# Optimization experiments

Measured on AMD Instinct MI355X. Metric: run time of the kernel, lower is better.

Reference implementation:

```python
import jax, jax.numpy as jnp
import numpy as np

D = 256  # hardcoded Dense units in the original layer

def setup_inputs() -> dict:
    key = jax.random.key(0)
    ks = jax.random.split(key, 7)
    B, S, F = 8, 2048, 256
    x = jax.random.normal(ks[0], (B, S, F), dtype=jnp.float32)
    # Dense layers (kernel + bias), glorot-ish scale
    scale = 1.0 / np.sqrt(F)
    Wq = jax.random.normal(ks[1], (F, D), dtype=jnp.float32) * scale
    Wk = jax.random.normal(ks[2], (F, D), dtype=jnp.float32) * scale
    Wv = jax.random.normal(ks[3], (F, D), dtype=jnp.float32) * scale
    bq = jax.random.normal(ks[4], (D,), dtype=jnp.float32) * 0.01
    bk = jax.random.normal(ks[5], (D,), dtype=jnp.float32) * 0.01
    bv = jax.random.normal(ks[6], (D,), dtype=jnp.float32) * 0.01
    return {"x": x, "Wq": Wq, "bq": bq, "Wk": Wk, "bk": bk, "Wv": Wv, "bv": bv}

def reference(x, Wq, bq, Wk, bk, Wv, bv):
    # Q/K/V projections: Dense(256) == x @ W + b
    Q = jnp.einsum('bsf,fd->bsd', x, Wq) + bq
    K = jnp.einsum('bsf,fd->bsd', x, Wk) + bk
    V = jnp.einsum('bsf,fd->bsd', x, Wv) + bv
    scores = jnp.einsum('bqd,bkd->bqk', Q, K) / jnp.sqrt(jnp.float32(D))
    attn = jax.nn.softmax(scores, axis=-1)
    return jnp.einsum('bqk,bkd->bqd', attn, V)
```

## Files before the change

kernel.cpp:

```cpp
#include <hip/hip_runtime.h>

typedef __bf16 bf16;
typedef __bf16 bf16x4v __attribute__((ext_vector_type(4)));
typedef __bf16 bf16x8 __attribute__((ext_vector_type(8)));
typedef float f32x4 __attribute__((ext_vector_type(4)));
typedef short s16x4 __attribute__((ext_vector_type(4)));

#define MFMA_X32(A, B, C) __builtin_amdgcn_mfma_f32_16x16x32_bf16(A, B, C, 0, 0, 0)

#if __has_builtin(__builtin_amdgcn_mfma_f32_16x16x16_bf16)
static __device__ __forceinline__ f32x4 mfma_x16(bf16x4v a, bf16x4v b, f32x4 c) {
  return __builtin_amdgcn_mfma_f32_16x16x16_bf16(a, b, c, 0, 0, 0);
}
#else
static __device__ __forceinline__ f32x4 mfma_x16(bf16x4v a, bf16x4v b, f32x4 c) {
  return __builtin_amdgcn_mfma_f32_16x16x16bf16_1k(
      __builtin_bit_cast(s16x4, a), __builtin_bit_cast(s16x4, b), c, 0, 0, 0);
}
#endif

static __device__ __forceinline__ float fast_exp2(float x) {
  float r;
  asm volatile("v_exp_f32 %0, %1\n\ts_nop 0" : "=v"(r) : "v"(x));
  return r;
}

static __device__ __forceinline__ void gll16(const void* g, void* l) {
  __builtin_amdgcn_global_load_lds(
      (const __attribute__((address_space(1))) void*)g,
      (__attribute__((address_space(3))) void*)l, 16, 0, 0);
}

#define WT_OFF 0
#define Q_OFF 393216
#define K_OFF 8781824
#define V_OFF 17170432

__global__ __launch_bounds__(256) void prep_wt(const float* __restrict__ Wq,
                                               const float* __restrict__ Wk,
                                               const float* __restrict__ Wv,
                                               bf16* __restrict__ Wt) {
  const int idx = blockIdx.x * 256 + threadIdx.x;
  const int p = idx >> 16;
  const int rem = idx & 65535;
  const int k = rem >> 8, n = rem & 255;
  const float* W = (p == 0) ? Wq : ((p == 1) ? Wk : Wv);
  Wt[p * 65536 + n * 256 + k] = (bf16)W[rem];
}

__global__ __launch_bounds__(256, 3) void proj_qkv(const float* __restrict__ x,
                                                   const float* __restrict__ bq,
                                                   const float* __restrict__ bk,
                                                   const float* __restrict__ bv,
                                                   char* __restrict__ ws0) {
  __shared__ __align__(16) char smem[40960];
  const bf16* Wt = (const bf16*)(ws0 + WT_OFF);
  bf16* Qo = (bf16*)(ws0 + Q_OFF);
  bf16* Ko = (bf16*)(ws0 + K_OFF);
  bf16* Vc = (bf16*)(ws0 + V_OFF);
  const int t = threadIdx.x;
  const int lane = t & 63, w = t >> 6, l16 = lane & 15, quad = lane >> 4;
  const int fam = blockIdx.x % 6;
  const int rgroup = blockIdx.x / 6;
  const int p = fam >> 1, ch = fam & 1;
  const float* bias = (p == 0) ? bq : ((p == 1) ? bk : bv);
  const float sc = (p == 0) ? 0.09016844005556021f : 1.0f;

  const int nl = w * 32 + l16;
  bf16x8 bfr[2][8];
#pragma unroll
  for (int nt = 0; nt < 2; ++nt)
#pragma unroll
    for (int kt = 0; kt < 8; ++kt)
      bfr[nt][kt] = *(const bf16x8*)&Wt[p * 65536 + (ch * 128 + nl + nt * 16) * 256 +
                                        kt * 32 + quad * 8];
  float bias2[2];
#pragma unroll
  for (int nt = 0; nt < 2; ++nt) bias2[nt] = bias[ch * 128 + nl + nt * 16];

  const int row0 = rgroup * 128;
  char* outL = smem + 32768;

  float4 xr[4][2];
#define STAGE_LOAD(tile)                                                        \
  {                                                                             \
    const float* xp = x + (row0 + (tile) * 32) * 256;                           \
    _Pragma("unroll") for (int i = 0; i < 4; ++i) {                             \
      const int u2 = i * 256 + t, row = u2 >> 5, col8 = (u2 & 31) * 8;          \
      xr[i][0] = *(const float4*)&xp[row * 256 + col8];                         \
      xr[i][1] = *(const float4*)&xp[row * 256 + col8 + 4];                     \
    }                                                                           \
  }
#define STAGE_WRITE(buf)                                                        \
  {                                                                             \
    _Pragma("unroll") for (int i = 0; i < 4; ++i) {                             \
      const int u2 = i * 256 + t, row = u2 >> 5, col8 = (u2 & 31) * 8;          \
      const float* f0 = (const float*)&xr[i][0];                                \
      const float* f1 = (const float*)&xr[i][1];                                \
      bf16x8 h;                                                                 \
      _Pragma("unroll") for (int j = 0; j < 4; ++j) {                           \
        h[j] = (bf16)f0[j];                                                     \
        h[4 + j] = (bf16)f1[j];                                                 \
      }                                                                         \
      *(bf16x8*)&smem[(buf) * 16384 + row * 512 +                               \
                      ((col8 * 2) ^ ((row & 7) << 4))] = h;                     \
    }                                                                           \
  }

  STAGE_LOAD(0);
  STAGE_WRITE(0);
  __syncthreads();

  int cur = 0;
  for (int tt = 0; tt < 4; ++tt) {
    if (tt < 3) STAGE_LOAD(tt + 1);

    f32x4 acc[2][2];
#pragma unroll
    for (int rs = 0; rs < 2; ++rs)
#pragma unroll
      for (int nt = 0; nt < 2; ++nt) acc[rs][nt] = f32x4{0.f, 0.f, 0.f, 0.f};
    const char* xb = smem + cur * 16384;
#pragma unroll
    for (int rs = 0; rs < 2; ++rs) {
      const int row = rs * 16 + l16;
#pragma unroll
      for (int kt = 0; kt < 8; ++kt) {
        const bf16x8 a = *(const bf16x8*)(xb + row * 512 +
                                          ((kt * 64 + quad * 16) ^ ((l16 & 7) << 4)));
        acc[rs][0] = MFMA_X32(a, bfr[0][kt], acc[rs][0]);
        acc[rs][1] = MFMA_X32(a, bfr[1][kt], acc[rs][1]);
      }
    }
    __syncthreads();

#pragma unroll
    for (int rs = 0; rs < 2; ++rs)
#pragma unroll
      for (int nt = 0; nt < 2; ++nt)
#pragma unroll
        for (int r = 0; r < 4; ++r) {
          const int sl = rs * 16 + quad * 4 + r;
          const int nn = nl + nt * 16;
          const bf16 hv = (bf16)((acc[rs][nt][r] + bias2[nt]) * sc);
          int pos;
          if (p == 0)
            pos = sl * 128 + nn;
          else if (p == 1)
            pos = (sl >> 4) * 2048 + (nn >> 5) * 512 + ((nn >> 3) & 3) * 128 +
                  (sl & 15) * 8 + (nn & 7);
          else
            pos = (sl >> 4) * 2048 + (nn >> 4) * 256 + ((sl & 15) >> 2) * 64 +
                  (nn & 15) * 4 + (sl & 3);
          *(bf16*)(outL + pos * 2) = hv;
        }
    if (tt < 3) STAGE_WRITE(cur ^ 1);
    __syncthreads();

    const int rowg = row0 + tt * 32;
    if (p == 0) {
      const int row = t >> 3, cb = (t & 7) * 32;
      const float4 v0 = *(const float4*)(outL + row * 256 + cb);
      const float4 v1 = *(const float4*)(outL + row * 256 + cb + 16);
      char* dst = (char*)Qo + (rowg + row) * 512 + ch * 256 + cb;
      *(float4*)dst = v0;
      *(float4*)(dst + 16) = v1;
    } else {
      const int b2 = rowg >> 11, s0 = rowg & 2047;
      bf16* O = (p == 1) ? Ko : Vc;
      char* dst = (char*)O + b2 * 1048576 + ((s0 >> 4) + (t >> 7)) * 8192 +
                  ch * 4096 + (t & 127) * 32;
      const float4 v0 = *(const float4*)(outL + t * 32);
      const float4 v1 = *(const float4*)(outL + t * 32 + 16);
      *(float4*)dst = v0;
      *(float4*)(dst + 16) = v1;
    }
    cur ^= 1;
  }
#undef STAGE_LOAD
#undef STAGE_WRITE
}

#define BUF_SZ 65536
#define SLOT_SZ 16640

__global__ __launch_bounds__(512, 2) void flash_attn(const char* __restrict__ ws0,
                                                     float* __restrict__ out) {
  __shared__ __align__(1024) char smem[135168];
  const bf16* Qp = (const bf16*)(ws0 + Q_OFF);
  const int t = threadIdx.x;
  const int lane = t & 63, w = t >> 6;
  const int l16 = lane & 15, quad = lane >> 4;
  const int qs = w & 1, kq = w >> 1;
  const int b = blockIdx.x & 7;
  const int qt = blockIdx.x >> 3;
  const int qrow0 = b * 2048 + qt * 64 + qs * 32;

  bf16x8 qf[2][8];
#pragma unroll
  for (int qsub = 0; qsub < 2; ++qsub)
#pragma unroll
    for (int kt = 0; kt < 8; ++kt)
      qf[qsub][kt] =
          *(const bf16x8*)&Qp[(qrow0 + qsub * 16 + l16) * 256 + kt * 32 + quad * 8];

  f32x4 o[2][16];
#pragma unroll
  for (int qsub = 0; qsub < 2; ++qsub)
#pragma unroll
    for (int dt = 0; dt < 16; ++dt) o[qsub][dt] = f32x4{0.f, 0.f, 0.f, 0.f};
  float m_[2] = {-1e30f, -1e30f}, l_[2] = {0.f, 0.f};

  unsigned goff[8], loff[8];
#pragma unroll
  for (int i = 0; i < 8; ++i) {
    const int u = w * 8 + i;
    const int kq2 = (u & 31) >> 3, e = u & 7;
    goff[i] = (u < 32 ? (unsigned)K_OFF : (unsigned)V_OFF) + b * 1048576u +
              kq2 * 262144u + e * 1024u + lane * 16u;
    loff[i] = kq2 * 16384u + (u < 32 ? 0u : 8192u) + e * 1024u;
  }
#pragma unroll
  for (int i = 0; i < 8; ++i) gll16(ws0 + goff[i], smem + loff[i]);

  for (int it = 0; it < 32; ++it) {
    __syncthreads();
    const unsigned cur = (unsigned)(it & 1) * BUF_SZ;
    if (it + 1 < 32) {
      const unsigned nxt = (unsigned)((it + 1) & 1) * BUF_SZ;
      const unsigned gadd = (unsigned)(it + 1) * 8192u;
#pragma unroll
      for (int i = 0; i < 8; ++i) gll16(ws0 + goff[i] + gadd, smem + nxt + loff[i]);
    }

    const char* kb = smem + cur + kq * 16384 + lane * 16;
    f32x4 s0 = f32x4{0.f, 0.f, 0.f, 0.f}, s1 = s0;
#pragma unroll
    for (int kt = 0; kt < 8; ++kt) {
      const bf16x8 kf = *(const bf16x8*)(kb + kt * 1024);
      s0 = MFMA_X32(kf, qf[0][kt], s0);
      s1 = MFMA_X32(kf, qf[1][kt], s1);
    }

    bf16x4v pa[2];
#pragma unroll
    for (int qsub = 0; qsub < 2; ++qsub) {
      const f32x4 s = qsub ? s1 : s0;
      float cm = fmaxf(fmaxf(s[0], s[1]), fmaxf(s[2], s[3]));
      cm = fmaxf(cm, __shfl_xor(cm, 16));
      cm = fmaxf(cm, __shfl_xor(cm, 32));
      const float mold = m_[qsub];
      const float mnew = fmaxf(mold, cm);
      bf16x4v pp;
      float ps = 0.f;
#pragma unroll
      for (int r = 0; r < 4; ++r) {
        const float e = fast_exp2(s[r] - mnew);
        const bf16 pb = (bf16)e;
        pp[r] = pb;
        ps += (float)pb;
      }
      ps += __shfl_xor(ps, 16);
      ps += __shfl_xor(ps, 32);
      if (__any(mnew > mold)) {
        const float al = fast_exp2(mold - mnew);
        m_[qsub] = mnew;
        l_[qsub] = l_[qsub] * al + ps;
        float ar[4];
#pragma unroll
        for (int r = 0; r < 4; ++r)
          ar[r] = __shfl(al, (quad << 4) + (quad << 2) + r);
#pragma unroll
        for (int dt = 0; dt < 16; ++dt)
#pragma unroll
          for (int r = 0; r < 4; ++r) o[qsub][dt][r] *= ar[r];
      } else {
        l_[qsub] += ps;
      }
      pa[qsub] = pp;
    }

    const char* vb = smem + cur + kq * 16384 + 8192 + lane * 8;
#pragma unroll
    for (int dt = 0; dt < 16; ++dt) {
      const bf16x4v vf = *(const bf16x4v*)(vb + dt * 512);
      o[0][dt] = mfma_x16(pa[0], vf, o[0][dt]);
      o[1][dt] = mfma_x16(pa[1], vf, o[1][dt]);
    }
  }

  float* mlf = (float*)(smem + 133120);
  if (quad == 0) {
#pragma unroll
    for (int qsub = 0; qsub < 2; ++qsub) {
      const int base = ((kq * 2 + qs) * 2 + qsub) * 32;
      mlf[base + l16] = m_[qsub];
      mlf[base + 16 + l16] = l_[qsub];
    }
  }
  __syncthreads();
#pragma unroll
  for (int qsub = 0; qsub < 2; ++qsub) {
    float M = -1e30f, mk[4], lk[4];
#pragma unroll
    for (int k2 = 0; k2 < 4; ++k2) {
      const int base = ((k2 * 2 + qs) * 2 + qsub) * 32;
      mk[k2] = mlf[base + l16];
      lk[k2] = mlf[base + 16 + l16];
      M = fmaxf(M, mk[k2]);
    }
    float L = 0.f;
#pragma unroll
    for (int k2 = 0; k2 < 4; ++k2) L += lk[k2] * fast_exp2(mk[k2] - M);
    const float sg = fast_exp2(m_[qsub] - M) / L;
    float sr[4];
#pragma unroll
    for (int r = 0; r < 4; ++r) sr[r] = __shfl(sg, (quad << 4) + (quad << 2) + r);
#pragma unroll
    for (int dt = 0; dt < 16; ++dt)
#pragma unroll
      for (int r = 0; r < 4; ++r) o[qsub][dt][r] *= sr[r];
  }
  if (kq >= 2) {
#pragma unroll
    for (int qsub = 0; qsub < 2; ++qsub) {
      float* sb = (float*)(smem + ((kq - 2) * 4 + qs * 2 + qsub) * SLOT_SZ);
#pragma unroll
      for (int dt = 0; dt < 16; ++dt)
#pragma unroll
        for (int r = 0; r < 4; ++r)
          sb[(quad * 4 + r) * 260 + dt * 16 + l16] = o[qsub][dt][r];
    }
  }
  __syncthreads();
  if (kq < 2) {
#pragma unroll
    for (int qsub = 0; qsub < 2; ++qsub) {
      const float* sb = (const float*)(smem + (kq * 4 + qs * 2 + qsub) * SLOT_SZ);
#pragma unroll
      for (int dt = 0; dt < 16; ++dt)
#pragma unroll
        for (int r = 0; r < 4; ++r)
          o[qsub][dt][r] += sb[(quad * 4 + r) * 260 + dt * 16 + l16];
    }
  }
  __syncthreads();
  if (kq == 1) {
#pragma unroll
    for (int qsub = 0; qsub < 2; ++qsub) {
      float* sb = (float*)(smem + (qs * 2 + qsub) * SLOT_SZ);
#pragma unroll
      for (int dt = 0; dt < 16; ++dt)
#pragma unroll
        for (int r = 0; r < 4; ++r)
          sb[(quad * 4 + r) * 260 + dt * 16 + l16] = o[qsub][dt][r];
    }
  }
  __syncthreads();
  if (kq == 0) {
#pragma unroll
    for (int qsub = 0; qsub < 2; ++qsub) {
      const float* sb = (const float*)(smem + (qs * 2 + qsub) * SLOT_SZ);
#pragma unroll
      for (int dt = 0; dt < 16; ++dt)
#pragma unroll
        for (int r = 0; r < 4; ++r) {
          const float v = o[qsub][dt][r] + sb[(quad * 4 + r) * 260 + dt * 16 + l16];
          out[(qrow0 + qsub * 16 + quad * 4 + r) * 256 + dt * 16 + l16] = v;
        }
    }
  }
}

extern "C" void kernel_launch(void* const* d_in, const int* in_sizes, int n_in,
                              void* d_out, int out_size, void* d_ws,
                              size_t ws_size, hipStream_t stream) {
  const float* x = (const float*)d_in[0];
  const float* Wq = (const float*)d_in[1];
  const float* bq = (const float*)d_in[2];
  const float* Wk = (const float*)d_in[3];
  const float* bk = (const float*)d_in[4];
  const float* Wv = (const float*)d_in[5];
  const float* bv = (const float*)d_in[6];
  float* out = (float*)d_out;
  char* ws = (char*)d_ws;

  prep_wt<<<768, 256, 0, stream>>>(Wq, Wk, Wv, (bf16*)(ws + WT_OFF));
  proj_qkv<<<768, 256, 0, stream>>>(x, bq, bk, bv, ws);
  flash_attn<<<256, 512, 0, stream>>>(ws, out);
}
```

Baseline: 177.2 us.

## Split flash-attn work across 16 waves with one 16-row query tile each

The attention block grows from 512 to 1024 threads. Each wave now owns a single 16-row query sub-tile instead of two, which halves the per-thread Q fragments and output accumulators, and each wave issues half as many async K/V loads. The change also raises MFMA instruction priority with s_setprio around the QK and PV loops. The aim is more waves in flight to hide latency, at the cost of half the MFMA reuse of each loaded K/V fragment per wave and more barrier participants. LDS per block is unchanged at about 132 KB, so still only one block fits per CU.

```diff
diff --git a/kernel.cpp b/kernel.cpp
--- a/kernel.cpp
+++ b/kernel.cpp
@@ -184,44 +184,39 @@
 #define BUF_SZ 65536
 #define SLOT_SZ 16640
 
-__global__ __launch_bounds__(512, 2) void flash_attn(const char* __restrict__ ws0,
-                                                     float* __restrict__ out) {
+__global__ __launch_bounds__(1024, 4) void flash_attn(const char* __restrict__ ws0,
+                                                      float* __restrict__ out) {
   __shared__ __align__(1024) char smem[135168];
   const bf16* Qp = (const bf16*)(ws0 + Q_OFF);
   const int t = threadIdx.x;
   const int lane = t & 63, w = t >> 6;
   const int l16 = lane & 15, quad = lane >> 4;
-  const int qs = w & 1, kq = w >> 1;
+  const int qw = w & 3, kq = w >> 2;
   const int b = blockIdx.x & 7;
   const int qt = blockIdx.x >> 3;
-  const int qrow0 = b * 2048 + qt * 64 + qs * 32;
-
-  bf16x8 qf[2][8];
-#pragma unroll
-  for (int qsub = 0; qsub < 2; ++qsub)
-#pragma unroll
-    for (int kt = 0; kt < 8; ++kt)
-      qf[qsub][kt] =
-          *(const bf16x8*)&Qp[(qrow0 + qsub * 16 + l16) * 256 + kt * 32 + quad * 8];
-
-  f32x4 o[2][16];
-#pragma unroll
-  for (int qsub = 0; qsub < 2; ++qsub)
-#pragma unroll
-    for (int dt = 0; dt < 16; ++dt) o[qsub][dt] = f32x4{0.f, 0.f, 0.f, 0.f};
-  float m_[2] = {-1e30f, -1e30f}, l_[2] = {0.f, 0.f};
-
-  unsigned goff[8], loff[8];
-#pragma unroll
-  for (int i = 0; i < 8; ++i) {
-    const int u = w * 8 + i;
+  const int qrow0 = b * 2048 + qt * 64;
+
+  bf16x8 qf[8];
+#pragma unroll
+  for (int kt = 0; kt < 8; ++kt)
+    qf[kt] = *(const bf16x8*)&Qp[(qrow0 + qw * 16 + l16) * 256 + kt * 32 + quad * 8];
+
+  f32x4 o[16];
+#pragma unroll
+  for (int dt = 0; dt < 16; ++dt) o[dt] = f32x4{0.f, 0.f, 0.f, 0.f};
+  float m_ = -1e30f, l_ = 0.f;
+
+  unsigned goff[4], loff[4];
+#pragma unroll
+  for (int i = 0; i < 4; ++i) {
+    const int u = w * 4 + i;
     const int kq2 = (u & 31) >> 3, e = u & 7;
     goff[i] = (u < 32 ? (unsigned)K_OFF : (unsigned)V_OFF) + b * 1048576u +
               kq2 * 262144u + e * 1024u + lane * 16u;
     loff[i] = kq2 * 16384u + (u < 32 ? 0u : 8192u) + e * 1024u;
   }
 #pragma unroll
-  for (int i = 0; i < 8; ++i) gll16(ws0 + goff[i], smem + loff[i]);
+  for (int i = 0; i < 4; ++i) gll16(ws0 + goff[i], smem + loff[i]);
 
   for (int it = 0; it < 32; ++it) {
     __syncthreads();
@@ -230,81 +225,73 @@
       const unsigned nxt = (unsigned)((it + 1) & 1) * BUF_SZ;
       const unsigned gadd = (unsigned)(it + 1) * 8192u;
 #pragma unroll
-      for (int i = 0; i < 8; ++i) gll16(ws0 + goff[i] + gadd, smem + nxt + loff[i]);
+      for (int i = 0; i < 4; ++i) gll16(ws0 + goff[i] + gadd, smem + nxt + loff[i]);
     }
 
     const char* kb = smem + cur + kq * 16384 + lane * 16;
-    f32x4 s0 = f32x4{0.f, 0.f, 0.f, 0.f}, s1 = s0;
+    f32x4 s0 = f32x4{0.f, 0.f, 0.f, 0.f};
+    __builtin_amdgcn_s_setprio(1);
 #pragma unroll
     for (int kt = 0; kt < 8; ++kt) {
       const bf16x8 kf = *(const bf16x8*)(kb + kt * 1024);
-      s0 = MFMA_X32(kf, qf[0][kt], s0);
-      s1 = MFMA_X32(kf, qf[1][kt], s1);
-    }
-
-    bf16x4v pa[2];
-#pragma unroll
-    for (int qsub = 0; qsub < 2; ++qsub) {
-      const f32x4 s = qsub ? s1 : s0;
-      float cm = fmaxf(fmaxf(s[0], s[1]), fmaxf(s[2], s[3]));
-      cm = fmaxf(cm, __shfl_xor(cm, 16));
-      cm = fmaxf(cm, __shfl_xor(cm, 32));
-      const float mold = m_[qsub];
-      const float mnew = fmaxf(mold, cm);
-      bf16x4v pp;
-      float ps = 0.f;
-#pragma unroll
-      for (int r = 0; r < 4; ++r) {
-        const float e = fast_exp2(s[r] - mnew);
-        const bf16 pb = (bf16)e;
-        pp[r] = pb;
-        ps += (float)pb;
-      }
-      ps += __shfl_xor(ps, 16);
-      ps += __shfl_xor(ps, 32);
-      if (__any(mnew > mold)) {
-        const float al = fast_exp2(mold - mnew);
-        m_[qsub] = mnew;
-        l_[qsub] = l_[qsub] * al + ps;
-        float ar[4];
-#pragma unroll
-        for (int r = 0; r < 4; ++r)
-          ar[r] = __shfl(al, (quad << 4) + (quad << 2) + r);
-#pragma unroll
-        for (int dt = 0; dt < 16; ++dt)
-#pragma unroll
-          for (int r = 0; r < 4; ++r) o[qsub][dt][r] *= ar[r];
-      } else {
-        l_[qsub] += ps;
-      }
-      pa[qsub] = pp;
+      s0 = MFMA_X32(kf, qf[kt], s0);
+    }
+    __builtin_amdgcn_s_setprio(0);
+
+    float cm = fmaxf(fmaxf(s0[0], s0[1]), fmaxf(s0[2], s0[3]));
+    cm = fmaxf(cm, __shfl_xor(cm, 16));
+    cm = fmaxf(cm, __shfl_xor(cm, 32));
+    const float mold = m_;
+    const float mnew = fmaxf(mold, cm);
+    bf16x4v pa;
+    float ps = 0.f;
+#pragma unroll
+    for (int r = 0; r < 4; ++r) {
+      const float e = fast_exp2(s0[r] - mnew);
+      const bf16 pb = (bf16)e;
+      pa[r] = pb;
+      ps += (float)pb;
+    }
+    ps += __shfl_xor(ps, 16);
+    ps += __shfl_xor(ps, 32);
+    if (__any(mnew > mold)) {
+      const float al = fast_exp2(mold - mnew);
+      m_ = mnew;
+      l_ = l_ * al + ps;
+      float ar[4];
+#pragma unroll
+      for (int r = 0; r < 4; ++r)
+        ar[r] = __shfl(al, (quad << 4) + (quad << 2) + r);
+#pragma unroll
+      for (int dt = 0; dt < 16; ++dt)
+#pragma unroll
+        for (int r = 0; r < 4; ++r) o[dt][r] *= ar[r];
+    } else {
+      l_ += ps;
     }
 
     const char* vb = smem + cur + kq * 16384 + 8192 + lane * 8;
+    __builtin_amdgcn_s_setprio(1);
 #pragma unroll
     for (int dt = 0; dt < 16; ++dt) {
       const bf16x4v vf = *(const bf16x4v*)(vb + dt * 512);
-      o[0][dt] = mfma_x16(pa[0], vf, o[0][dt]);
-      o[1][dt] = mfma_x16(pa[1], vf, o[1][dt]);
-    }
+      o[dt] = mfma_x16(pa, vf, o[dt]);
+    }
+    __builtin_amdgcn_s_setprio(0);
   }
 
   float* mlf = (float*)(smem + 133120);
   if (quad == 0) {
-#pragma unroll
-    for (int qsub = 0; qsub < 2; ++qsub) {
-      const int base = ((kq * 2 + qs) * 2 + qsub) * 32;
-      mlf[base + l16] = m_[qsub];
-      mlf[base + 16 + l16] = l_[qsub];
-    }
-  }
-  __syncthreads();
-#pragma unroll
-  for (int qsub = 0; qsub < 2; ++qsub) {
+    const int base = (kq * 4 + qw) * 32;
+    mlf[base + l16] = m_;
+    mlf[base + 16 + l16] = l_;
+  }
+  __syncthreads();
+  {
     float M = -1e30f, mk[4], lk[4];
 #pragma unroll
     for (int k2 = 0; k2 < 4; ++k2) {
-      const int base = ((k2 * 2 + qs) * 2 + qsub) * 32;
+      const int base = (k2 * 4 + qw) * 32;
       mk[k2] = mlf[base + l16];
       lk[k2] = mlf[base + 16 + l16];
       M = fmaxf(M, mk[k2]);
@@ -312,63 +299,51 @@
     float L = 0.f;
 #pragma unroll
     for (int k2 = 0; k2 < 4; ++k2) L += lk[k2] * fast_exp2(mk[k2] - M);
-    const float sg = fast_exp2(m_[qsub] - M) / L;
+    const float sg = fast_exp2(m_ - M) / L;
     float sr[4];
 #pragma unroll
     for (int r = 0; r < 4; ++r) sr[r] = __shfl(sg, (quad << 4) + (quad << 2) + r);
 #pragma unroll
     for (int dt = 0; dt < 16; ++dt)
 #pragma unroll
-      for (int r = 0; r < 4; ++r) o[qsub][dt][r] *= sr[r];
+      for (int r = 0; r < 4; ++r) o[dt][r] *= sr[r];
   }
   if (kq >= 2) {
-#pragma unroll
-    for (int qsub = 0; qsub < 2; ++qsub) {
-      float* sb = (float*)(smem + ((kq - 2) * 4 + qs * 2 + qsub) * SLOT_SZ);
-#pragma unroll
-      for (int dt = 0; dt < 16; ++dt)
-#pragma unroll
-        for (int r = 0; r < 4; ++r)
-          sb[(quad * 4 + r) * 260 + dt * 16 + l16] = o[qsub][dt][r];
-    }
+    float* sb = (float*)(smem + ((kq - 2) * 4 + qw) * SLOT_SZ);
+#pragma unroll
+    for (int dt = 0; dt < 16; ++dt)
+#pragma unroll
+      for (int r = 0; r < 4; ++r)
+        sb[(quad * 4 + r) * 260 + dt * 16 + l16] = o[dt][r];
   }
   __syncthreads();
   if (kq < 2) {
-#pragma unroll
-    for (int qsub = 0; qsub < 2; ++qsub) {
-      const float* sb = (const float*)(smem + (kq * 4 + qs * 2 + qsub) * SLOT_SZ);
-#pragma unroll
-      for (int dt = 0; dt < 16; ++dt)
-#pragma unroll
-        for (int r = 0; r < 4; ++r)
-          o[qsub][dt][r] += sb[(quad * 4 + r) * 260 + dt * 16 + l16];
-    }
+    const float* sb = (const float*)(smem + (kq * 4 + qw) * SLOT_SZ);
+#pragma unroll
+    for (int dt = 0; dt < 16; ++dt)
+#pragma unroll
+      for (int r = 0; r < 4; ++r)
+        o[dt][r] += sb[(quad * 4 + r) * 260 + dt * 16 + l16];
   }
   __syncthreads();
   if (kq == 1) {
-#pragma unroll
-    for (int qsub = 0; qsub < 2; ++qsub) {
-      float* sb = (float*)(smem + (qs * 2 + qsub) * SLOT_SZ);
-#pragma unroll
-      for (int dt = 0; dt < 16; ++dt)
-#pragma unroll
-        for (int r = 0; r < 4; ++r)
-          sb[(quad * 4 + r) * 260 + dt * 16 + l16] = o[qsub][dt][r];
-    }
+    float* sb = (float*)(smem + qw * SLOT_SZ);
+#pragma unroll
+    for (int dt = 0; dt < 16; ++dt)
+#pragma unroll
+      for (int r = 0; r < 4; ++r)
+        sb[(quad * 4 + r) * 260 + dt * 16 + l16] = o[dt][r];
   }
   __syncthreads();
   if (kq == 0) {
-#pragma unroll
-    for (int qsub = 0; qsub < 2; ++qsub) {
-      const float* sb = (const float*)(smem + (qs * 2 + qsub) * SLOT_SZ);
-#pragma unroll
-      for (int dt = 0; dt < 16; ++dt)
-#pragma unroll
-        for (int r = 0; r < 4; ++r) {
-          const float v = o[qsub][dt][r] + sb[(quad * 4 + r) * 260 + dt * 16 + l16];
-          out[(qrow0 + qsub * 16 + quad * 4 + r) * 256 + dt * 16 + l16] = v;
-        }
-    }
+    const float* sb = (const float*)(smem + qw * SLOT_SZ);
+#pragma unroll
+    for (int dt = 0; dt < 16; ++dt)
+#pragma unroll
+      for (int r = 0; r < 4; ++r) {
+        const float v = o[dt][r] + sb[(quad * 4 + r) * 260 + dt * 16 + l16];
+        out[(qrow0 + qw * 16 + quad * 4 + r) * 256 + dt * 16 + l16] = v;
+      }
   }
 }
 
@@ -387,5 +362,5 @@
 
   prep_wt<<<768, 256, 0, stream>>>(Wq, Wk, Wv, (bf16*)(ws + WT_OFF));
   proj_qkv<<<768, 256, 0, stream>>>(x, bq, bk, bv, ws);
-  flash_attn<<<256, 512, 0, stream>>>(ws, out);
-}
+  flash_attn<<<256, 1024, 0, stream>>>(ws, out);
+}
```

Result: no change. 176.0 us (-0.7%).

## Stage only K through LDS, read V directly from global, double key block

Applied to the files above, without the earlier changes.

The attention loop now streams only K tiles into shared memory, 32 keys per wave per iteration across 16 iterations instead of 16 keys across 32. V fragments are loaded straight from global memory (relying on cache) rather than via LDS. The change also raises wave priority around the QK MFMA block and removes the padding from the reduction slots, which shrinks LDS use. Fewer barriers and a larger MFMA batch per iteration are traded for uncached-latency V loads on the critical path and possible LDS bank conflicts in the unpadded reduction.

```diff
diff --git a/kernel.cpp b/kernel.cpp
--- a/kernel.cpp
+++ b/kernel.cpp
@@ -182,11 +182,11 @@
 }
 
 #define BUF_SZ 65536
-#define SLOT_SZ 16640
+#define SLOT_SZ 16384
 
 __global__ __launch_bounds__(512, 2) void flash_attn(const char* __restrict__ ws0,
                                                      float* __restrict__ out) {
-  __shared__ __align__(1024) char smem[135168];
+  __shared__ __align__(1024) char smem[133120];
   const bf16* Qp = (const bf16*)(ws0 + Q_OFF);
   const int t = threadIdx.x;
   const int lane = t & 63, w = t >> 6;
@@ -215,50 +215,64 @@
 #pragma unroll
   for (int i = 0; i < 8; ++i) {
     const int u = w * 8 + i;
-    const int kq2 = (u & 31) >> 3, e = u & 7;
-    goff[i] = (u < 32 ? (unsigned)K_OFF : (unsigned)V_OFF) + b * 1048576u +
-              kq2 * 262144u + e * 1024u + lane * 16u;
-    loff[i] = kq2 * 16384u + (u < 32 ? 0u : 8192u) + e * 1024u;
+    const int kq2 = u >> 4, rem = u & 15;
+    const int half = rem >> 3, e = rem & 7;
+    goff[i] = (unsigned)K_OFF + b * 1048576u + (kq2 * 32 + half) * 8192u +
+              e * 1024u + lane * 16u;
+    loff[i] = kq2 * 16384u + half * 8192u + e * 1024u;
   }
 #pragma unroll
   for (int i = 0; i < 8; ++i) gll16(ws0 + goff[i], smem + loff[i]);
 
-  for (int it = 0; it < 32; ++it) {
+  const char* vg0 = ws0 + V_OFF + (unsigned)b * 1048576u + (unsigned)kq * 262144u +
+                    (unsigned)lane * 8u;
+
+  for (int it = 0; it < 16; ++it) {
     __syncthreads();
     const unsigned cur = (unsigned)(it & 1) * BUF_SZ;
-    if (it + 1 < 32) {
+    if (it + 1 < 16) {
       const unsigned nxt = (unsigned)((it + 1) & 1) * BUF_SZ;
-      const unsigned gadd = (unsigned)(it + 1) * 8192u;
+      const unsigned gadd = (unsigned)(it + 1) * 16384u;
 #pragma unroll
       for (int i = 0; i < 8; ++i) gll16(ws0 + goff[i] + gadd, smem + nxt + loff[i]);
     }
 
     const char* kb = smem + cur + kq * 16384 + lane * 16;
-    f32x4 s0 = f32x4{0.f, 0.f, 0.f, 0.f}, s1 = s0;
+    f32x4 s[2][2];
+#pragma unroll
+    for (int qsub = 0; qsub < 2; ++qsub)
+#pragma unroll
+      for (int kc = 0; kc < 2; ++kc) s[qsub][kc] = f32x4{0.f, 0.f, 0.f, 0.f};
+    __builtin_amdgcn_s_setprio(1);
 #pragma unroll
     for (int kt = 0; kt < 8; ++kt) {
-      const bf16x8 kf = *(const bf16x8*)(kb + kt * 1024);
-      s0 = MFMA_X32(kf, qf[0][kt], s0);
-      s1 = MFMA_X32(kf, qf[1][kt], s1);
-    }
-
-    bf16x4v pa[2];
-#pragma unroll
-    for (int qsub = 0; qsub < 2; ++qsub) {
-      const f32x4 s = qsub ? s1 : s0;
-      float cm = fmaxf(fmaxf(s[0], s[1]), fmaxf(s[2], s[3]));
+      const bf16x8 kf0 = *(const bf16x8*)(kb + kt * 1024);
+      const bf16x8 kf1 = *(const bf16x8*)(kb + 8192 + kt * 1024);
+      s[0][0] = MFMA_X32(kf0, qf[0][kt], s[0][0]);
+      s[0][1] = MFMA_X32(kf1, qf[0][kt], s[0][1]);
+      s[1][0] = MFMA_X32(kf0, qf[1][kt], s[1][0]);
+      s[1][1] = MFMA_X32(kf1, qf[1][kt], s[1][1]);
+    }
+    __builtin_amdgcn_s_setprio(0);
+
+    bf16x4v pa[2][2];
+#pragma unroll
+    for (int qsub = 0; qsub < 2; ++qsub) {
+      const f32x4 sA = s[qsub][0], sB = s[qsub][1];
+      float cm = fmaxf(fmaxf(fmaxf(sA[0], sA[1]), fmaxf(sA[2], sA[3])),
+                       fmaxf(fmaxf(sB[0], sB[1]), fmaxf(sB[2], sB[3])));
       cm = fmaxf(cm, __shfl_xor(cm, 16));
       cm = fmaxf(cm, __shfl_xor(cm, 32));
       const float mold = m_[qsub];
       const float mnew = fmaxf(mold, cm);
-      bf16x4v pp;
       float ps = 0.f;
 #pragma unroll
       for (int r = 0; r < 4; ++r) {
-        const float e = fast_exp2(s[r] - mnew);
-        const bf16 pb = (bf16)e;
-        pp[r] = pb;
-        ps += (float)pb;
+        const bf16 p0 = (bf16)fast_exp2(sA[r] - mnew);
+        const bf16 p1 = (bf16)fast_exp2(sB[r] - mnew);
+        pa[qsub][0][r] = p0;
+        pa[qsub][1][r] = p1;
+        ps += (float)p0 + (float)p1;
       }
       ps += __shfl_xor(ps, 16);
       ps += __shfl_xor(ps, 32);
@@ -277,19 +291,21 @@
       } else {
         l_[qsub] += ps;
       }
-      pa[qsub] = pp;
-    }
-
-    const char* vb = smem + cur + kq * 16384 + 8192 + lane * 8;
+    }
+
+    const char* vg = vg0 + (unsigned)it * 16384u;
 #pragma unroll
     for (int dt = 0; dt < 16; ++dt) {
-      const bf16x4v vf = *(const bf16x4v*)(vb + dt * 512);
-      o[0][dt] = mfma_x16(pa[0], vf, o[0][dt]);
-      o[1][dt] = mfma_x16(pa[1], vf, o[1][dt]);
-    }
-  }
-
-  float* mlf = (float*)(smem + 133120);
+      const bf16x4v va = *(const bf16x4v*)(vg + dt * 512);
+      const bf16x4v vb = *(const bf16x4v*)(vg + 8192 + dt * 512);
+      o[0][dt] = mfma_x16(pa[0][0], va, o[0][dt]);
+      o[0][dt] = mfma_x16(pa[0][1], vb, o[0][dt]);
+      o[1][dt] = mfma_x16(pa[1][0], va, o[1][dt]);
+      o[1][dt] = mfma_x16(pa[1][1], vb, o[1][dt]);
+    }
+  }
+
+  float* mlf = (float*)(smem + 131072);
   if (quad == 0) {
 #pragma unroll
     for (int qsub = 0; qsub < 2; ++qsub) {
@@ -329,7 +345,7 @@
       for (int dt = 0; dt < 16; ++dt)
 #pragma unroll
         for (int r = 0; r < 4; ++r)
-          sb[(quad * 4 + r) * 260 + dt * 16 + l16] = o[qsub][dt][r];
+          sb[(quad * 4 + r) * 256 + dt * 16 + l16] = o[qsub][dt][r];
     }
   }
   __syncthreads();
@@ -341,7 +357,7 @@
       for (int dt = 0; dt < 16; ++dt)
 #pragma unroll
         for (int r = 0; r < 4; ++r)
-          o[qsub][dt][r] += sb[(quad * 4 + r) * 260 + dt * 16 + l16];
+          o[qsub][dt][r] += sb[(quad * 4 + r) * 256 + dt * 16 + l16];
     }
   }
   __syncthreads();
@@ -353,7 +369,7 @@
       for (int dt = 0; dt < 16; ++dt)
 #pragma unroll
         for (int r = 0; r < 4; ++r)
-          sb[(quad * 4 + r) * 260 + dt * 16 + l16] = o[qsub][dt][r];
+          sb[(quad * 4 + r) * 256 + dt * 16 + l16] = o[qsub][dt][r];
     }
   }
   __syncthreads();
@@ -365,7 +381,7 @@
       for (int dt = 0; dt < 16; ++dt)
 #pragma unroll
         for (int r = 0; r < 4; ++r) {
-          const float v = o[qsub][dt][r] + sb[(quad * 4 + r) * 260 + dt * 16 + l16];
+          const float v = o[qsub][dt][r] + sb[(quad * 4 + r) * 256 + dt * 16 + l16];
           out[(qrow0 + qsub * 16 + quad * 4 + r) * 256 + dt * 16 + l16] = v;
         }
     }
```

Result: slower. 221.1 us (+24.8%).

## Process two key tiles per iteration with K32 MFMA for PV and lazy rescaling

Applied to the files above, without the earlier changes.

The attention loop now handles 32 keys per iteration: two K tiles with separate double-buffered staging, and a single-buffered V tile whose layout is changed in the projection kernel. This allows the P·V product to use the 16x16x32 bf16 MFMA instead of 16x16x16, halving the number of PV MFMA issues. The running-max rescale of the output accumulator is skipped unless the max grows by more than 6 (log2 units), and s_setprio hints are placed around the MFMA sections. It trades a wider exponent range in unnormalised P and a more intricate barrier and staging schedule for fewer rescales and fewer MFMA issues.

```diff
diff --git a/kernel.cpp b/kernel.cpp
--- a/kernel.cpp
+++ b/kernel.cpp
@@ -7,17 +7,6 @@
 typedef short s16x4 __attribute__((ext_vector_type(4)));
 
 #define MFMA_X32(A, B, C) __builtin_amdgcn_mfma_f32_16x16x32_bf16(A, B, C, 0, 0, 0)
-
-#if __has_builtin(__builtin_amdgcn_mfma_f32_16x16x16_bf16)
-static __device__ __forceinline__ f32x4 mfma_x16(bf16x4v a, bf16x4v b, f32x4 c) {
-  return __builtin_amdgcn_mfma_f32_16x16x16_bf16(a, b, c, 0, 0, 0);
-}
-#else
-static __device__ __forceinline__ f32x4 mfma_x16(bf16x4v a, bf16x4v b, f32x4 c) {
-  return __builtin_amdgcn_mfma_f32_16x16x16bf16_1k(
-      __builtin_bit_cast(s16x4, a), __builtin_bit_cast(s16x4, b), c, 0, 0, 0);
-}
-#endif
 
 static __device__ __forceinline__ float fast_exp2(float x) {
   float r;
@@ -150,8 +139,8 @@
             pos = (sl >> 4) * 2048 + (nn >> 5) * 512 + ((nn >> 3) & 3) * 128 +
                   (sl & 15) * 8 + (nn & 7);
           else
-            pos = (sl >> 4) * 2048 + (nn >> 4) * 256 + ((sl & 15) >> 2) * 64 +
-                  (nn & 15) * 4 + (sl & 3);
+            pos = (nn >> 4) * 512 + ((sl >> 2) & 3) * 128 + (nn & 15) * 8 +
+                  (sl >> 4) * 4 + (sl & 3);
           *(bf16*)(outL + pos * 2) = hv;
         }
     if (tt < 3) STAGE_WRITE(cur ^ 1);
@@ -165,15 +154,21 @@
       char* dst = (char*)Qo + (rowg + row) * 512 + ch * 256 + cb;
       *(float4*)dst = v0;
       *(float4*)(dst + 16) = v1;
-    } else {
+    } else if (p == 1) {
       const int b2 = rowg >> 11, s0 = rowg & 2047;
-      bf16* O = (p == 1) ? Ko : Vc;
-      char* dst = (char*)O + b2 * 1048576 + ((s0 >> 4) + (t >> 7)) * 8192 +
+      char* dst = (char*)Ko + b2 * 1048576 + ((s0 >> 4) + (t >> 7)) * 8192 +
                   ch * 4096 + (t & 127) * 32;
       const float4 v0 = *(const float4*)(outL + t * 32);
       const float4 v1 = *(const float4*)(outL + t * 32 + 16);
       *(float4*)dst = v0;
       *(float4*)(dst + 16) = v1;
+    } else {
+      const int b2 = rowg >> 11, s0 = rowg & 2047;
+      char* dst = (char*)Vc + b2 * 1048576 + (s0 >> 5) * 16384 + ch * 8192 + t * 32;
+      const float4 v0 = *(const float4*)(outL + t * 32);
+      const float4 v1 = *(const float4*)(outL + t * 32 + 16);
+      *(float4*)dst = v0;
+      *(float4*)(dst + 16) = v1;
     }
     cur ^= 1;
   }
@@ -181,7 +176,6 @@
 #undef STAGE_WRITE
 }
 
-#define BUF_SZ 65536
 #define SLOT_SZ 16640
 
 __global__ __launch_bounds__(512, 2) void flash_attn(const char* __restrict__ ws0,
@@ -211,60 +205,90 @@
     for (int dt = 0; dt < 16; ++dt) o[qsub][dt] = f32x4{0.f, 0.f, 0.f, 0.f};
   float m_[2] = {-1e30f, -1e30f}, l_[2] = {0.f, 0.f};
 
-  unsigned goff[8], loff[8];
+  unsigned goffK[4], loffK[4];
+#pragma unroll
+  for (int i = 0; i < 4; ++i) {
+    const int u = w * 4 + i;
+    const int kq2 = u >> 3, e = u & 7;
+    goffK[i] = (unsigned)K_OFF + b * 1048576u + kq2 * 262144u + e * 1024u + lane * 16u;
+    loffK[i] = kq2 * 8192u + e * 1024u;
+  }
+  unsigned goffV[8], loffV[8];
 #pragma unroll
   for (int i = 0; i < 8; ++i) {
     const int u = w * 8 + i;
-    const int kq2 = (u & 31) >> 3, e = u & 7;
-    goff[i] = (u < 32 ? (unsigned)K_OFF : (unsigned)V_OFF) + b * 1048576u +
-              kq2 * 262144u + e * 1024u + lane * 16u;
-    loff[i] = kq2 * 16384u + (u < 32 ? 0u : 8192u) + e * 1024u;
-  }
-#pragma unroll
-  for (int i = 0; i < 8; ++i) gll16(ws0 + goff[i], smem + loff[i]);
-
-  for (int it = 0; it < 32; ++it) {
+    const int kqv = u >> 4, e = u & 15;
+    goffV[i] = (unsigned)V_OFF + b * 1048576u + kqv * 262144u + e * 1024u + lane * 16u;
+    loffV[i] = 65536u + kqv * 16384u + e * 1024u;
+  }
+
+#define STAGE_K(S)                                                             \
+  {                                                                            \
+    _Pragma("unroll") for (int i = 0; i < 4; ++i)                              \
+        gll16(ws0 + goffK[i] + (unsigned)(S) * 8192u,                          \
+              smem + (unsigned)(((S) & 1) * 32768) + loffK[i]);                \
+  }
+#define STAGE_V(P)                                                             \
+  {                                                                            \
+    _Pragma("unroll") for (int i = 0; i < 8; ++i)                              \
+        gll16(ws0 + goffV[i] + (unsigned)(P) * 16384u, smem + loffV[i]);       \
+  }
+#define QK_STEP(CURK, KC)                                                      \
+  {                                                                            \
+    const char* kb = smem + (CURK) + kq * 8192 + lane * 16;                    \
+    __builtin_amdgcn_s_setprio(1);                                             \
+    _Pragma("unroll") for (int kt = 0; kt < 8; ++kt) {                         \
+      const bf16x8 kf = *(const bf16x8*)(kb + kt * 1024);                      \
+      sfr[0][KC] = MFMA_X32(kf, qf[0][kt], sfr[0][KC]);                        \
+      sfr[1][KC] = MFMA_X32(kf, qf[1][kt], sfr[1][KC]);                        \
+    }                                                                          \
+    __builtin_amdgcn_s_setprio(0);                                             \
+  }
+
+  STAGE_K(0);
+
+  for (int p = 0; p < 16; ++p) {
+    f32x4 sfr[2][2];
+#pragma unroll
+    for (int qsub = 0; qsub < 2; ++qsub)
+#pragma unroll
+      for (int kc = 0; kc < 2; ++kc) sfr[qsub][kc] = f32x4{0.f, 0.f, 0.f, 0.f};
+
     __syncthreads();
-    const unsigned cur = (unsigned)(it & 1) * BUF_SZ;
-    if (it + 1 < 32) {
-      const unsigned nxt = (unsigned)((it + 1) & 1) * BUF_SZ;
-      const unsigned gadd = (unsigned)(it + 1) * 8192u;
-#pragma unroll
-      for (int i = 0; i < 8; ++i) gll16(ws0 + goff[i] + gadd, smem + nxt + loff[i]);
-    }
-
-    const char* kb = smem + cur + kq * 16384 + lane * 16;
-    f32x4 s0 = f32x4{0.f, 0.f, 0.f, 0.f}, s1 = s0;
-#pragma unroll
-    for (int kt = 0; kt < 8; ++kt) {
-      const bf16x8 kf = *(const bf16x8*)(kb + kt * 1024);
-      s0 = MFMA_X32(kf, qf[0][kt], s0);
-      s1 = MFMA_X32(kf, qf[1][kt], s1);
-    }
-
-    bf16x4v pa[2];
-#pragma unroll
-    for (int qsub = 0; qsub < 2; ++qsub) {
-      const f32x4 s = qsub ? s1 : s0;
-      float cm = fmaxf(fmaxf(s[0], s[1]), fmaxf(s[2], s[3]));
+    STAGE_K(2 * p + 1);
+    STAGE_V(p);
+    QK_STEP((unsigned)((2 * p) & 1) * 32768u, 0);
+
+    __syncthreads();
+    if (p < 15) STAGE_K(2 * p + 2);
+    QK_STEP((unsigned)((2 * p + 1) & 1) * 32768u, 1);
+
+    bf16x8 pa[2];
+#pragma unroll
+    for (int qsub = 0; qsub < 2; ++qsub) {
+      const f32x4 sA = sfr[qsub][0], sB = sfr[qsub][1];
+      float cm = fmaxf(fmaxf(fmaxf(sA[0], sA[1]), fmaxf(sA[2], sA[3])),
+                       fmaxf(fmaxf(sB[0], sB[1]), fmaxf(sB[2], sB[3])));
       cm = fmaxf(cm, __shfl_xor(cm, 16));
       cm = fmaxf(cm, __shfl_xor(cm, 32));
       const float mold = m_[qsub];
-      const float mnew = fmaxf(mold, cm);
-      bf16x4v pp;
+      const bool upd = __any(cm > mold + 6.0f);
+      float Mref = mold;
+      if (upd) Mref = fmaxf(mold, cm);
       float ps = 0.f;
 #pragma unroll
       for (int r = 0; r < 4; ++r) {
-        const float e = fast_exp2(s[r] - mnew);
-        const bf16 pb = (bf16)e;
-        pp[r] = pb;
-        ps += (float)pb;
+        const bf16 p0 = (bf16)fast_exp2(sA[r] - Mref);
+        const bf16 p1 = (bf16)fast_exp2(sB[r] - Mref);
+        pa[qsub][r] = p0;
+        pa[qsub][4 + r] = p1;
+        ps += (float)p0 + (float)p1;
       }
       ps += __shfl_xor(ps, 16);
       ps += __shfl_xor(ps, 32);
-      if (__any(mnew > mold)) {
-        const float al = fast_exp2(mold - mnew);
-        m_[qsub] = mnew;
+      if (upd) {
+        const float al = fast_exp2(mold - Mref);
+        m_[qsub] = Mref;
         l_[qsub] = l_[qsub] * al + ps;
         float ar[4];
 #pragma unroll
@@ -277,17 +301,21 @@
       } else {
         l_[qsub] += ps;
       }
-      pa[qsub] = pp;
-    }
-
-    const char* vb = smem + cur + kq * 16384 + 8192 + lane * 8;
+    }
+
+    const char* vb = smem + 65536 + kq * 16384 + lane * 16;
+    __builtin_amdgcn_s_setprio(1);
 #pragma unroll
     for (int dt = 0; dt < 16; ++dt) {
-      const bf16x4v vf = *(const bf16x4v*)(vb + dt * 512);
-      o[0][dt] = mfma_x16(pa[0], vf, o[0][dt]);
-      o[1][dt] = mfma_x16(pa[1], vf, o[1][dt]);
-    }
-  }
+      const bf16x8 vf = *(const bf16x8*)(vb + dt * 1024);
+      o[0][dt] = MFMA_X32(pa[0], vf, o[0][dt]);
+      o[1][dt] = MFMA_X32(pa[1], vf, o[1][dt]);
+    }
+    __builtin_amdgcn_s_setprio(0);
+  }
+#undef STAGE_K
+#undef STAGE_V
+#undef QK_STEP
 
   float* mlf = (float*)(smem + 133120);
   if (quad == 0) {
```

Result: faster. 164.0 us (-7.4%).
